# Kernel tuning notes

Measured on AMD Instinct MI355X. Metric: run time of the kernel, lower is better.

Reference implementation:

```python
import jax, jax.numpy as jnp
import numpy as np

N = 8_000_000  # number of (parent, child, relation) edges
N_RELS = 64
P = 3  # n_polarities


def sparsemax(z):
    # sparsemax along last axis (Martins & Astudillo 2016)
    d = z.shape[-1]
    zs = jnp.sort(z, axis=-1)[..., ::-1]          # descending
    cs = jnp.cumsum(zs, axis=-1)
    k = jnp.arange(1, d + 1, dtype=z.dtype)
    support = 1.0 + k * zs > cs                   # [.., d] bool
    ksup = jnp.sum(support, axis=-1, keepdims=True)  # int, size of support
    tau = (jnp.take_along_axis(cs, ksup - 1, axis=-1) - 1.0) / ksup.astype(z.dtype)
    return jnp.maximum(z - tau, 0.0)


def setup_inputs() -> dict:
    key = jax.random.key(0)
    k1, k2, k3, k4, k5 = jax.random.split(key, 5)
    prnt_probs = jax.random.uniform(k1, (N, P), dtype=jnp.float32)
    child_probs = jax.random.uniform(k2, (N, P), dtype=jnp.float32)
    rels = jax.random.randint(k3, (N,), 0, N_RELS, dtype=jnp.int32)
    # learned params (torch inits to ones/constants; perturb so grads are non-degenerate)
    M = 1.0 + 0.1 * jax.random.normal(k4, (N_RELS, P, P), dtype=jnp.float32)
    beta = jax.random.uniform(k5, (N_RELS, P), dtype=jnp.float32)
    z_epsilon = jnp.float32(0.01)
    scale_factor = jnp.float32(21.0)
    return {"prnt_probs": prnt_probs, "child_probs": child_probs, "M": M,
            "beta": beta, "z_epsilon": z_epsilon, "scale_factor": scale_factor,
            "rels": rels, "var_sfx": 0}


def reference(prnt_probs, child_probs, M, beta, z_epsilon, scale_factor, rels, var_sfx):
    # All rows of child_probs/prnt_probs are nonzero (uniform fill), so the
    # nonzero() gathers select every edge and the copy branch is empty:
    # this is the dense alpha path of AlphaModel.forward.
    c = jnp.einsum('nij,nj->ni', M[rels], child_probs)  # relation-gated bmm
    c = sparsemax(c)
    c = sparsemax(c)  # alpha branch re-applies sparsemax (idempotent but faithful)
    p = sparsemax(prnt_probs)
    b = beta[rels]
    alpha = (1.0 - b) * p + b * c
    # scale(): entropy of clamped mixture + cosine similarity
    z = jnp.maximum(p + c, jax.lax.stop_gradient(z_epsilon))  # torch uses .item() -> no grad
    z = z / jnp.sum(z, axis=-1, keepdims=True)
    entropy = -jnp.sum(z * jnp.log(z), axis=-1)
    cos = jnp.sum(p * c, axis=-1)
    norm = jnp.maximum(jnp.linalg.norm(p, axis=-1) * jnp.linalg.norm(c, axis=-1), 1e-10)
    cos = 0.1 + cos / norm
    scale = scale_factor * cos / entropy
    alpha = jnp.maximum(alpha * scale[:, None], 0.001)
    return alpha
```

## Files before the change

kernel.cpp:

```cpp
#include <hip/hip_runtime.h>

#define BLOCK 256

__device__ __forceinline__ float fast_ln(float x) {
    return 0.69314718056f * __builtin_amdgcn_logf(x);
}
__device__ __forceinline__ float fast_rcp(float x) {
    return __builtin_amdgcn_rcpf(x);
}
__device__ __forceinline__ float fast_rsq(float x) {
    return __builtin_amdgcn_rsqf(x);
}

__device__ __forceinline__ float bperm(int ab, float v) {
    return __int_as_float(__builtin_amdgcn_ds_bpermute(ab, __float_as_int(v)));
}

__device__ __forceinline__ void sparsemax3(float z0, float z1, float z2,
                                           float& o0, float& o1, float& o2) {
    float lo01 = fminf(z0, z1), hi01 = fmaxf(z0, z1);
    float s2 = fminf(lo01, z2);
    float mx = fmaxf(lo01, z2);
    float s0 = fmaxf(hi01, mx);
    float s1 = fminf(hi01, mx);
    float cs2 = s0 + s1;
    float cs3 = cs2 + s2;
    bool k2 = (1.0f + 2.0f * s1 > cs2);
    bool k3 = (1.0f + 3.0f * s2 > cs3);
    int k = 1 + (int)k2 + (int)k3;
    float csk = (k == 1) ? s0 : ((k == 2) ? cs2 : cs3);
    float rk  = (k == 1) ? 1.0f : ((k == 2) ? 0.5f : 0.33333334f);
    float tau = (csk - 1.0f) * rk;
    o0 = fmaxf(z0 - tau, 0.0f);
    o1 = fmaxf(z1 - tau, 0.0f);
    o2 = fmaxf(z2 - tau, 0.0f);
}

__device__ __forceinline__ void edge_core(
    float p0, float p1, float p2,
    float q0, float q1, float q2,
    float m00, float m01, float m02,
    float m10, float m11, float m12,
    float m20, float m21, float m22,
    float b0, float b1, float b2,
    float zeps, float sf,
    float& a0o, float& a1o, float& a2o)
{
    float c0 = m00 * q0 + m01 * q1 + m02 * q2;
    float c1 = m10 * q0 + m11 * q1 + m12 * q2;
    float c2 = m20 * q0 + m21 * q1 + m22 * q2;
    sparsemax3(c0, c1, c2, c0, c1, c2);
    sparsemax3(p0, p1, p2, p0, p1, p2);
    float a0 = p0 + b0 * (c0 - p0);
    float a1 = p1 + b1 * (c1 - p1);
    float a2 = p2 + b2 * (c2 - p2);
    float z0 = fmaxf(p0 + c0, zeps);
    float z1 = fmaxf(p1 + c1, zeps);
    float z2 = fmaxf(p2 + c2, zeps);
    float rs = fast_rcp(z0 + z1 + z2);
    z0 *= rs; z1 *= rs; z2 *= rs;
    float ent = -(z0 * fast_ln(z0) + z1 * fast_ln(z1) + z2 * fast_ln(z2));
    float dot = p0 * c0 + p1 * c1 + p2 * c2;
    float pp = p0 * p0 + p1 * p1 + p2 * p2;
    float cc = c0 * c0 + c1 * c1 + c2 * c2;
    float cosv = 0.1f + dot * fast_rsq(fmaxf(pp * cc, 1e-20f));
    float scale = sf * cosv * fast_rcp(ent);
    a0o = fmaxf(a0 * scale, 0.001f);
    a1o = fmaxf(a1 * scale, 0.001f);
    a2o = fmaxf(a2 * scale, 0.001f);
}

__global__ __launch_bounds__(BLOCK) void alpha_kernel(
    const float* __restrict__ prnt, const float* __restrict__ child,
    const float* __restrict__ Mg, const float* __restrict__ betag,
    const float* __restrict__ zeps_p, const float* __restrict__ sf_p,
    const int* __restrict__ rels, float* __restrict__ out, int n_edges)
{
    const int lane = threadIdx.x & 63;
    float mt[9], bt[3];
    {
        const float* mr = Mg + lane * 9;
#pragma unroll
        for (int k = 0; k < 9; ++k) mt[k] = mr[k];
        const float* br = betag + lane * 3;
#pragma unroll
        for (int k = 0; k < 3; ++k) bt[k] = br[k];
    }

    const float zeps = zeps_p[0];
    const float sf   = sf_p[0];
    const int nt4 = n_edges >> 2;
    const int t = blockIdx.x * BLOCK + threadIdx.x;

    if (nt4 > 0) {
        const int tc = min(t, nt4 - 1);
        const float4* p4 = (const float4*)prnt;
        const float4* c4 = (const float4*)child;
        int4 r4 = ((const int4*)rels)[tc];
        float4 pa = p4[3 * tc + 0], pb = p4[3 * tc + 1], pc = p4[3 * tc + 2];
        float4 ca = c4[3 * tc + 0], cb = c4[3 * tc + 1], cc = c4[3 * tc + 2];
        float P[12] = {pa.x, pa.y, pa.z, pa.w, pb.x, pb.y, pb.z, pb.w,
                       pc.x, pc.y, pc.z, pc.w};
        float C[12] = {ca.x, ca.y, ca.z, ca.w, cb.x, cb.y, cb.z, cb.w,
                       cc.x, cc.y, cc.z, cc.w};
        int R[4] = {r4.x, r4.y, r4.z, r4.w};
        float O[12];
#pragma unroll
        for (int e = 0; e < 4; ++e) {
            int ab = R[e] << 2;
            float g0 = bperm(ab, mt[0]), g1 = bperm(ab, mt[1]), g2 = bperm(ab, mt[2]);
            float g3 = bperm(ab, mt[3]), g4 = bperm(ab, mt[4]), g5 = bperm(ab, mt[5]);
            float g6 = bperm(ab, mt[6]), g7 = bperm(ab, mt[7]), g8 = bperm(ab, mt[8]);
            float h0 = bperm(ab, bt[0]), h1 = bperm(ab, bt[1]), h2 = bperm(ab, bt[2]);
            edge_core(P[3 * e], P[3 * e + 1], P[3 * e + 2],
                      C[3 * e], C[3 * e + 1], C[3 * e + 2],
                      g0, g1, g2, g3, g4, g5, g6, g7, g8,
                      h0, h1, h2, zeps, sf,
                      O[3 * e], O[3 * e + 1], O[3 * e + 2]);
        }
        if (t < nt4) {
            float4* o4 = (float4*)out;
            float4 oa = {O[0], O[1], O[2],  O[3]};
            float4 ob = {O[4], O[5], O[6],  O[7]};
            float4 oc = {O[8], O[9], O[10], O[11]};
            o4[3 * t + 0] = oa;
            o4[3 * t + 1] = ob;
            o4[3 * t + 2] = oc;
        }
        if (t == nt4) {
            for (int e = nt4 * 4; e < n_edges; ++e) {
                int r = rels[e];
                const float* m = Mg + r * 9;
                const float* b = betag + r * 3;
                float a0, a1, a2;
                edge_core(prnt[3 * e], prnt[3 * e + 1], prnt[3 * e + 2],
                          child[3 * e], child[3 * e + 1], child[3 * e + 2],
                          m[0], m[1], m[2], m[3], m[4], m[5], m[6], m[7], m[8],
                          b[0], b[1], b[2], zeps, sf, a0, a1, a2);
                out[3 * e] = a0; out[3 * e + 1] = a1; out[3 * e + 2] = a2;
            }
        }
    }
}

extern "C" void kernel_launch(void* const* d_in, const int* in_sizes, int n_in,
                              void* d_out, int out_size, void* d_ws, size_t ws_size,
                              hipStream_t stream) {
    const float* prnt  = (const float*)d_in[0];
    const float* child = (const float*)d_in[1];
    const float* Mg    = (const float*)d_in[2];
    const float* betag = (const float*)d_in[3];
    const float* zeps  = (const float*)d_in[4];
    const float* sf    = (const float*)d_in[5];
    const int*   rels  = (const int*)d_in[6];
    float* out = (float*)d_out;

    int n_edges = in_sizes[0] / 3;
    int nthreads = (n_edges >> 2) + 1;
    int nblocks = (nthreads + BLOCK - 1) / BLOCK;
    alpha_kernel<<<nblocks, BLOCK, 0, stream>>>(
        prnt, child, Mg, betag, zeps, sf, rels, out, n_edges);
}
```

Before: 265.5 us.

## Use persistent grid-stride loop with double-buffered register prefetch and nontemporal stores

Replaces the one-chunk-per-thread launch with a fixed grid of 2048 blocks that loop over chunks in grid-stride order. The next chunk's loads are issued into a second register set before the current chunk is computed, so memory latency overlaps compute. Output writes use nontemporal stores to avoid polluting cache. This also amortizes the per-thread M/beta table loads, but uses more registers and may lower occupancy.

```diff
diff --git a/kernel.cpp b/kernel.cpp
--- a/kernel.cpp
+++ b/kernel.cpp
@@ -1,6 +1,9 @@
 #include <hip/hip_runtime.h>
 
 #define BLOCK 256
+#define GRID  2048
+
+typedef float f32x4 __attribute__((ext_vector_type(4)));
 
 __device__ __forceinline__ float fast_ln(float x) {
     return 0.69314718056f * __builtin_amdgcn_logf(x);
@@ -90,55 +93,88 @@
     const float zeps = zeps_p[0];
     const float sf   = sf_p[0];
     const int nt4 = n_edges >> 2;
-    const int t = blockIdx.x * BLOCK + threadIdx.x;
 
     if (nt4 > 0) {
-        const int tc = min(t, nt4 - 1);
-        const float4* p4 = (const float4*)prnt;
-        const float4* c4 = (const float4*)child;
-        int4 r4 = ((const int4*)rels)[tc];
-        float4 pa = p4[3 * tc + 0], pb = p4[3 * tc + 1], pc = p4[3 * tc + 2];
-        float4 ca = c4[3 * tc + 0], cb = c4[3 * tc + 1], cc = c4[3 * tc + 2];
-        float P[12] = {pa.x, pa.y, pa.z, pa.w, pb.x, pb.y, pb.z, pb.w,
-                       pc.x, pc.y, pc.z, pc.w};
-        float C[12] = {ca.x, ca.y, ca.z, ca.w, cb.x, cb.y, cb.z, cb.w,
-                       cc.x, cc.y, cc.z, cc.w};
-        int R[4] = {r4.x, r4.y, r4.z, r4.w};
-        float O[12];
+        const int S  = GRID * BLOCK;
+        const int t0 = blockIdx.x * BLOCK + threadIdx.x;
+        const int iters = (nt4 + S - 1) / S;
+        const float4* p4  = (const float4*)prnt;
+        const float4* c4  = (const float4*)child;
+        const int4*   r4p = (const int4*)rels;
+        f32x4* o4 = reinterpret_cast<f32x4*>(out);
+
+        float4 Apa, Apb, Apc, Aca, Acb, Acc; int4 Ar;
+        float4 Bpa, Bpb, Bpc, Bca, Bcb, Bcc; int4 Br;
+
+        auto load_chunk = [&](int idx, float4& pa, float4& pb, float4& pc,
+                              float4& ca, float4& cb, float4& cc, int4& rr) {
+            rr = r4p[idx];
+            pa = p4[3 * idx + 0]; pb = p4[3 * idx + 1]; pc = p4[3 * idx + 2];
+            ca = c4[3 * idx + 0]; cb = c4[3 * idx + 1]; cc = c4[3 * idx + 2];
+        };
+
+        auto work_chunk = [&](int k, const float4& pa, const float4& pb,
+                              const float4& pc, const float4& ca,
+                              const float4& cb, const float4& cc,
+                              const int4& rr) {
+            float P[12] = {pa.x, pa.y, pa.z, pa.w, pb.x, pb.y, pb.z, pb.w,
+                           pc.x, pc.y, pc.z, pc.w};
+            float C[12] = {ca.x, ca.y, ca.z, ca.w, cb.x, cb.y, cb.z, cb.w,
+                           cc.x, cc.y, cc.z, cc.w};
+            int R[4] = {rr.x, rr.y, rr.z, rr.w};
+            float O[12];
 #pragma unroll
-        for (int e = 0; e < 4; ++e) {
-            int ab = R[e] << 2;
-            float g0 = bperm(ab, mt[0]), g1 = bperm(ab, mt[1]), g2 = bperm(ab, mt[2]);
-            float g3 = bperm(ab, mt[3]), g4 = bperm(ab, mt[4]), g5 = bperm(ab, mt[5]);
-            float g6 = bperm(ab, mt[6]), g7 = bperm(ab, mt[7]), g8 = bperm(ab, mt[8]);
-            float h0 = bperm(ab, bt[0]), h1 = bperm(ab, bt[1]), h2 = bperm(ab, bt[2]);
-            edge_core(P[3 * e], P[3 * e + 1], P[3 * e + 2],
-                      C[3 * e], C[3 * e + 1], C[3 * e + 2],
-                      g0, g1, g2, g3, g4, g5, g6, g7, g8,
-                      h0, h1, h2, zeps, sf,
-                      O[3 * e], O[3 * e + 1], O[3 * e + 2]);
+            for (int e = 0; e < 4; ++e) {
+                int ab = R[e] << 2;
+                float g0 = bperm(ab, mt[0]), g1 = bperm(ab, mt[1]), g2 = bperm(ab, mt[2]);
+                float g3 = bperm(ab, mt[3]), g4 = bperm(ab, mt[4]), g5 = bperm(ab, mt[5]);
+                float g6 = bperm(ab, mt[6]), g7 = bperm(ab, mt[7]), g8 = bperm(ab, mt[8]);
+                float h0 = bperm(ab, bt[0]), h1 = bperm(ab, bt[1]), h2 = bperm(ab, bt[2]);
+                edge_core(P[3 * e], P[3 * e + 1], P[3 * e + 2],
+                          C[3 * e], C[3 * e + 1], C[3 * e + 2],
+                          g0, g1, g2, g3, g4, g5, g6, g7, g8,
+                          h0, h1, h2, zeps, sf,
+                          O[3 * e], O[3 * e + 1], O[3 * e + 2]);
+            }
+            int i = t0 + k * S;
+            if (i < nt4) {
+                f32x4 oa = {O[0], O[1], O[2],  O[3]};
+                f32x4 ob = {O[4], O[5], O[6],  O[7]};
+                f32x4 oc = {O[8], O[9], O[10], O[11]};
+                __builtin_nontemporal_store(oa, &o4[3 * i + 0]);
+                __builtin_nontemporal_store(ob, &o4[3 * i + 1]);
+                __builtin_nontemporal_store(oc, &o4[3 * i + 2]);
+            }
+        };
+
+        load_chunk(min(t0, nt4 - 1), Apa, Apb, Apc, Aca, Acb, Acc, Ar);
+
+        for (int k = 0; k < iters; k += 2) {
+            const bool have1 = (k + 1 < iters);
+            if (have1)
+                load_chunk(min(t0 + (k + 1) * S, nt4 - 1),
+                           Bpa, Bpb, Bpc, Bca, Bcb, Bcc, Br);
+            work_chunk(k, Apa, Apb, Apc, Aca, Acb, Acc, Ar);
+            if (have1) {
+                if (k + 2 < iters)
+                    load_chunk(min(t0 + (k + 2) * S, nt4 - 1),
+                               Apa, Apb, Apc, Aca, Acb, Acc, Ar);
+                work_chunk(k + 1, Bpa, Bpb, Bpc, Bca, Bcb, Bcc, Br);
+            }
         }
-        if (t < nt4) {
-            float4* o4 = (float4*)out;
-            float4 oa = {O[0], O[1], O[2],  O[3]};
-            float4 ob = {O[4], O[5], O[6],  O[7]};
-            float4 oc = {O[8], O[9], O[10], O[11]};
-            o4[3 * t + 0] = oa;
-            o4[3 * t + 1] = ob;
-            o4[3 * t + 2] = oc;
-        }
-        if (t == nt4) {
-            for (int e = nt4 * 4; e < n_edges; ++e) {
-                int r = rels[e];
-                const float* m = Mg + r * 9;
-                const float* b = betag + r * 3;
-                float a0, a1, a2;
-                edge_core(prnt[3 * e], prnt[3 * e + 1], prnt[3 * e + 2],
-                          child[3 * e], child[3 * e + 1], child[3 * e + 2],
-                          m[0], m[1], m[2], m[3], m[4], m[5], m[6], m[7], m[8],
-                          b[0], b[1], b[2], zeps, sf, a0, a1, a2);
-                out[3 * e] = a0; out[3 * e + 1] = a1; out[3 * e + 2] = a2;
-            }
+    }
+
+    if (blockIdx.x == 0 && threadIdx.x == 0) {
+        for (int e = (n_edges >> 2) * 4; e < n_edges; ++e) {
+            int r = rels[e];
+            const float* m = Mg + r * 9;
+            const float* b = betag + r * 3;
+            float a0, a1, a2;
+            edge_core(prnt[3 * e], prnt[3 * e + 1], prnt[3 * e + 2],
+                      child[3 * e], child[3 * e + 1], child[3 * e + 2],
+                      m[0], m[1], m[2], m[3], m[4], m[5], m[6], m[7], m[8],
+                      b[0], b[1], b[2], zeps, sf, a0, a1, a2);
+            out[3 * e] = a0; out[3 * e + 1] = a1; out[3 * e + 2] = a2;
         }
     }
 }
@@ -156,8 +192,6 @@
     float* out = (float*)d_out;
 
     int n_edges = in_sizes[0] / 3;
-    int nthreads = (n_edges >> 2) + 1;
-    int nblocks = (nthreads + BLOCK - 1) / BLOCK;
-    alpha_kernel<<<nblocks, BLOCK, 0, stream>>>(
+    alpha_kernel<<<GRID, BLOCK, 0, stream>>>(
         prnt, child, Mg, betag, zeps, sf, rels, out, n_edges);
 }
```

New measurement: 283.9 us. +7.0%, slower.

## Stage prnt/child loads through LDS for coalesced reads and writes

Applied to the files above, without the earlier changes.

Replaces the per-thread strided float4 loads (three per array per thread at a 48-byte stride) with wave-cooperative global_load_lds transfers. Each lane fetches consecutive 16-byte chunks, then reads its 12-float slice back from LDS. Outputs are staged through the same LDS buffer and written out in contiguous 16-byte chunks per lane. The aim is fully coalesced global traffic, at the cost of 24 KB of LDS per block and the LDS round trips. The change also adds an occupancy hint to the launch bounds and moves the tail handling to thread 0 of block 0.

```diff
diff --git a/kernel.cpp b/kernel.cpp
--- a/kernel.cpp
+++ b/kernel.cpp
@@ -1,6 +1,9 @@
 #include <hip/hip_runtime.h>
 
 #define BLOCK 256
+#define NWAVES (BLOCK / 64)
+
+typedef float f32x4 __attribute__((ext_vector_type(4)));
 
 __device__ __forceinline__ float fast_ln(float x) {
     return 0.69314718056f * __builtin_amdgcn_logf(x);
@@ -14,6 +17,13 @@
 
 __device__ __forceinline__ float bperm(int ab, float v) {
     return __int_as_float(__builtin_amdgcn_ds_bpermute(ab, __float_as_int(v)));
+}
+
+__device__ __forceinline__ void gload_lds16(const float* g, float* l) {
+    __builtin_amdgcn_global_load_lds(
+        (const __attribute__((address_space(1))) unsigned int*)g,
+        (__attribute__((address_space(3))) unsigned int*)l,
+        16, 0, 0);
 }
 
 __device__ __forceinline__ void sparsemax3(float z0, float z1, float z2,
@@ -70,13 +80,19 @@
     a2o = fmaxf(a2 * scale, 0.001f);
 }
 
-__global__ __launch_bounds__(BLOCK) void alpha_kernel(
+__global__ __launch_bounds__(BLOCK, 6) void alpha_kernel(
     const float* __restrict__ prnt, const float* __restrict__ child,
     const float* __restrict__ Mg, const float* __restrict__ betag,
     const float* __restrict__ zeps_p, const float* __restrict__ sf_p,
     const int* __restrict__ rels, float* __restrict__ out, int n_edges)
 {
-    const int lane = threadIdx.x & 63;
+    __shared__ __align__(16) float sP[NWAVES * 768];
+    __shared__ __align__(16) float sC[NWAVES * 768];
+
+    const int tid  = threadIdx.x;
+    const int lane = tid & 63;
+    const int w    = tid >> 6;
+
     float mt[9], bt[3];
     {
         const float* mr = Mg + lane * 9;
@@ -90,15 +106,31 @@
     const float zeps = zeps_p[0];
     const float sf   = sf_p[0];
     const int nt4 = n_edges >> 2;
-    const int t = blockIdx.x * BLOCK + threadIdx.x;
+    const int t = blockIdx.x * BLOCK + tid;
 
     if (nt4 > 0) {
-        const int tc = min(t, nt4 - 1);
-        const float4* p4 = (const float4*)prnt;
-        const float4* c4 = (const float4*)child;
-        int4 r4 = ((const int4*)rels)[tc];
-        float4 pa = p4[3 * tc + 0], pb = p4[3 * tc + 1], pc = p4[3 * tc + 2];
-        float4 ca = c4[3 * tc + 0], cb = c4[3 * tc + 1], cc = c4[3 * tc + 2];
+        const int NT4F = 3 * nt4;
+        const int WB   = 3 * (blockIdx.x * BLOCK + (w << 6));
+        float* lp = &sP[w * 768];
+        float* lc = &sC[w * 768];
+
+#pragma unroll
+        for (int j = 0; j < 3; ++j) {
+            int g = min(WB + j * 64 + lane, NT4F - 1);
+            gload_lds16(prnt  + 4 * g, lp + j * 256);
+            gload_lds16(child + 4 * g, lc + j * 256);
+        }
+        int4 r4 = ((const int4*)rels)[min(t, nt4 - 1)];
+
+        asm volatile("s_waitcnt vmcnt(0)" ::: "memory");
+
+        f32x4 pa = *(const f32x4*)(lp + lane * 12);
+        f32x4 pb = *(const f32x4*)(lp + lane * 12 + 4);
+        f32x4 pc = *(const f32x4*)(lp + lane * 12 + 8);
+        f32x4 ca = *(const f32x4*)(lc + lane * 12);
+        f32x4 cb = *(const f32x4*)(lc + lane * 12 + 4);
+        f32x4 cc = *(const f32x4*)(lc + lane * 12 + 8);
+
         float P[12] = {pa.x, pa.y, pa.z, pa.w, pb.x, pb.y, pb.z, pb.w,
                        pc.x, pc.y, pc.z, pc.w};
         float C[12] = {ca.x, ca.y, ca.z, ca.w, cb.x, cb.y, cb.z, cb.w,
@@ -118,27 +150,33 @@
                       h0, h1, h2, zeps, sf,
                       O[3 * e], O[3 * e + 1], O[3 * e + 2]);
         }
-        if (t < nt4) {
-            float4* o4 = (float4*)out;
-            float4 oa = {O[0], O[1], O[2],  O[3]};
-            float4 ob = {O[4], O[5], O[6],  O[7]};
-            float4 oc = {O[8], O[9], O[10], O[11]};
-            o4[3 * t + 0] = oa;
-            o4[3 * t + 1] = ob;
-            o4[3 * t + 2] = oc;
-        }
-        if (t == nt4) {
-            for (int e = nt4 * 4; e < n_edges; ++e) {
-                int r = rels[e];
-                const float* m = Mg + r * 9;
-                const float* b = betag + r * 3;
-                float a0, a1, a2;
-                edge_core(prnt[3 * e], prnt[3 * e + 1], prnt[3 * e + 2],
-                          child[3 * e], child[3 * e + 1], child[3 * e + 2],
-                          m[0], m[1], m[2], m[3], m[4], m[5], m[6], m[7], m[8],
-                          b[0], b[1], b[2], zeps, sf, a0, a1, a2);
-                out[3 * e] = a0; out[3 * e + 1] = a1; out[3 * e + 2] = a2;
+
+        *(f32x4*)(lp + lane * 12)     = f32x4{O[0], O[1], O[2],  O[3]};
+        *(f32x4*)(lp + lane * 12 + 4) = f32x4{O[4], O[5], O[6],  O[7]};
+        *(f32x4*)(lp + lane * 12 + 8) = f32x4{O[8], O[9], O[10], O[11]};
+        asm volatile("s_waitcnt lgkmcnt(0)" ::: "memory");
+
+#pragma unroll
+        for (int j = 0; j < 3; ++j) {
+            int g = WB + j * 64 + lane;
+            if (g < NT4F) {
+                f32x4 v = *(const f32x4*)(lp + j * 256 + lane * 4);
+                *(f32x4*)(out + 4 * g) = v;
             }
+        }
+    }
+
+    if (blockIdx.x == 0 && threadIdx.x == 0) {
+        for (int e = (n_edges >> 2) * 4; e < n_edges; ++e) {
+            int r = rels[e];
+            const float* m = Mg + r * 9;
+            const float* b = betag + r * 3;
+            float a0, a1, a2;
+            edge_core(prnt[3 * e], prnt[3 * e + 1], prnt[3 * e + 2],
+                      child[3 * e], child[3 * e + 1], child[3 * e + 2],
+                      m[0], m[1], m[2], m[3], m[4], m[5], m[6], m[7], m[8],
+                      b[0], b[1], b[2], zeps, sf, a0, a1, a2);
+            out[3 * e] = a0; out[3 * e + 1] = a1; out[3 * e + 2] = a2;
         }
     }
 }
@@ -156,8 +194,9 @@
     float* out = (float*)d_out;
 
     int n_edges = in_sizes[0] / 3;
-    int nthreads = (n_edges >> 2) + 1;
-    int nblocks = (nthreads + BLOCK - 1) / BLOCK;
+    int nt4 = n_edges >> 2;
+    int nblocks = (nt4 + BLOCK - 1) / BLOCK;
+    if (nblocks < 1) nblocks = 1;
     alpha_kernel<<<nblocks, BLOCK, 0, stream>>>(
         prnt, child, Mg, betag, zeps, sf, rels, out, n_edges);
 }
```

Result: no change. 263.5 us (-0.8%).
